# Kernel optimization log

Hardware: AMD Instinct MI355X
Metric: run time of the kernel (lower is better)

The kernel has to match this reference:

```python
import jax, jax.numpy as jnp
import numpy as np

B = 1024
FEATS = [("sirna_gibbs_energy", 19), ("pssm_score", 1), ("gc_sterch", 1), ("sirna_second_percent", 2), ("sirna_second_energy", 2), ("tri_nt_percent", 64), ("di_nt_percent", 16), ("single_nt_percent", 4), ("gc_content", 1)]
DFF = 2048  # torch TransformerEncoderLayer default dim_feedforward


def _posenc(S, d):
    pos = jnp.arange(S, dtype=jnp.float32)[:, None]
    div = jnp.exp(jnp.arange(0, d, 2, dtype=jnp.float32) * (-np.log(10000.0) / d))
    pe = jnp.zeros((S, d), jnp.float32)
    pe = pe.at[:, 0::2].set(jnp.sin(pos * div))
    pe = pe.at[:, 1::2].set(jnp.cos(pos * div))
    return pe


def _ln(x, g, b):
    m = x.mean(-1, keepdims=True)
    v = ((x - m) ** 2).mean(-1, keepdims=True)
    return (x - m) * jax.lax.rsqrt(v + 1e-5) * g + b


def _encoder_layer(x, qkv_w, qkv_b, ow, ob, f1w, f1b, f2w, f2b, g1, b1, g2, b2, nhead):
    Bx, S, d = x.shape
    dh = d // nhead
    qkv = jnp.einsum('bsd,ed->bse', x, qkv_w) + qkv_b  # [B,S,3d]
    q, k, v = jnp.split(qkv, 3, axis=-1)
    sh = lambda t: t.reshape(Bx, S, nhead, dh).transpose(0, 2, 1, 3)  # [B,h,S,dh]
    q, k, v = sh(q), sh(k), sh(v)
    att = jax.nn.softmax(jnp.einsum('bhqd,bhkd->bhqk', q, k) / np.sqrt(dh).astype(np.float32), axis=-1)
    o = jnp.einsum('bhqk,bhkd->bhqd', att, v).transpose(0, 2, 1, 3).reshape(Bx, S, d)
    o = o @ ow.T + ob
    x = _ln(x + o, g1, b1)  # post-norm (norm_first=False default)
    h = jax.nn.relu(x @ f1w.T + f1b) @ f2w.T + f2b
    return _ln(x + h, g2, b2)


def _encoder(x, qkv_w, qkv_b, ow, ob, f1w, f1b, f2w, f2b, g1, b1, g2, b2, nhead):
    for i in range(qkv_w.shape[0]):
        x = _encoder_layer(x, qkv_w[i], qkv_b[i], ow[i], ob[i], f1w[i], f1b[i], f2w[i], f2b[i], g1[i], b1[i], g2[i], b2[i], nhead)
    return x


def setup_inputs():
    key = jax.random.key(0)
    ks = iter(jax.random.split(key, 128))
    inp = {}
    inp['rnafm_encode'] = jax.random.normal(next(ks), (B, 21, 640), jnp.float32)
    inp['rnafm_encode_mrna'] = jax.random.normal(next(ks), (B, 59, 640), jnp.float32)
    for name, n in FEATS:
        inp[name] = jax.random.normal(next(ks), (B, n, 1), jnp.float32)

    def xav(shape):
        fan_out, fan_in = shape[-2], shape[-1]
        std = np.sqrt(2.0 / (fan_in + fan_out)).astype(np.float32)
        return jax.random.normal(next(ks), shape, jnp.float32) * std

    def enc_params(prefix, L, d):
        inp[prefix + '_qkv_w'] = xav((L, 3 * d, d))
        inp[prefix + '_qkv_b'] = jnp.zeros((L, 3 * d), jnp.float32)
        inp[prefix + '_ow'] = xav((L, d, d))
        inp[prefix + '_ob'] = jnp.zeros((L, d), jnp.float32)
        inp[prefix + '_f1w'] = xav((L, DFF, d))
        inp[prefix + '_f1b'] = jnp.zeros((L, DFF), jnp.float32)
        inp[prefix + '_f2w'] = xav((L, d, DFF))
        inp[prefix + '_f2b'] = jnp.zeros((L, d), jnp.float32)
        inp[prefix + '_g1'] = jnp.ones((L, d), jnp.float32)
        inp[prefix + '_b1'] = jnp.zeros((L, d), jnp.float32)
        inp[prefix + '_g2'] = jnp.ones((L, d), jnp.float32)
        inp[prefix + '_b2'] = jnp.zeros((L, d), jnp.float32)

    inp['xmap1_w'] = xav((16, 640)); inp['xmap1_b'] = jnp.zeros(16, jnp.float32)
    enc_params('enc1', 4, 16)
    inp['ymap1_w'] = xav((4, 16)); inp['ymap1_b'] = jnp.zeros(4, jnp.float32)
    inp['xmap2_w'] = xav((8, 640)); inp['xmap2_b'] = jnp.zeros(8, jnp.float32)
    enc_params('enc2', 2, 8)
    inp['ymap2_w'] = xav((1, 8)); inp['ymap2_b'] = jnp.zeros(1, jnp.float32)
    inp['bn_g'] = jnp.ones(253, jnp.float32); inp['bn_b'] = jnp.zeros(253, jnp.float32)
    inp['d1w'] = xav((256, 253)); inp['d1b'] = jnp.zeros(256, jnp.float32)
    inp['d2w'] = xav((64, 256)); inp['d2b'] = jnp.zeros(64, jnp.float32)
    inp['d3w'] = xav((16, 64)); inp['d3b'] = jnp.zeros(16, jnp.float32)
    inp['d4w'] = xav((1, 16)); inp['d4b'] = jnp.zeros(1, jnp.float32)
    return inp


def _forward(rnafm_encode, rnafm_encode_mrna, feats,
             xmap1_w, xmap1_b, enc1, ymap1_w, ymap1_b,
             xmap2_w, xmap2_b, enc2, ymap2_w, ymap2_b,
             bn_g, bn_b, d1w, d1b, d2w, d2b, d3w, d3b, d4w, d4b):
    # siRNA branch: [B,21,640] -> [B,21,16] -> encoder(4 layers, 2 heads) -> [B,21,4]
    x = rnafm_encode @ xmap1_w.T + xmap1_b
    x = x + _posenc(21, 16)
    x = _encoder(x, *enc1, nhead=2)
    as_att = (x @ ymap1_w.T + ymap1_b).reshape(x.shape[0], -1)  # [B,84]
    # mRNA branch: [B,59,640] -> [B,59,8] -> encoder(2 layers, 1 head) -> [B,59,1]
    y = rnafm_encode_mrna @ xmap2_w.T + xmap2_b
    y = y + _posenc(59, 8)
    y = _encoder(y, *enc2, nhead=1)
    mrna_att = (y @ ymap2_w.T + ymap2_b).reshape(y.shape[0], -1)  # [B,59]
    other = jnp.concatenate([f[..., 0] for f in feats], axis=1)  # [B,110]
    cat = jnp.concatenate([as_att, mrna_att, other], axis=1)  # [B,253]
    # BatchNorm1d in eval mode (running_mean=0, running_var=1, eps=1e-5)
    h = cat * jax.lax.rsqrt(jnp.float32(1.0 + 1e-5)) * bn_g + bn_b
    h = jax.nn.leaky_relu(h @ d1w.T + d1b, 0.01)
    h = jax.nn.leaky_relu(h @ d2w.T + d2b, 0.01)
    h = jax.nn.leaky_relu(h @ d3w.T + d3b, 0.01)
    out = jax.nn.sigmoid(h @ d4w.T + d4b)
    return out[:, 0]


def reference(rnafm_encode, rnafm_encode_mrna, sirna_gibbs_energy, pssm_score, gc_sterch,
              sirna_second_percent, sirna_second_energy, tri_nt_percent, di_nt_percent,
              single_nt_percent, gc_content,
              xmap1_w, xmap1_b,
              enc1_qkv_w, enc1_qkv_b, enc1_ow, enc1_ob, enc1_f1w, enc1_f1b, enc1_f2w, enc1_f2b,
              enc1_g1, enc1_b1, enc1_g2, enc1_b2,
              ymap1_w, ymap1_b,
              xmap2_w, xmap2_b,
              enc2_qkv_w, enc2_qkv_b, enc2_ow, enc2_ob, enc2_f1w, enc2_f1b, enc2_f2w, enc2_f2b,
              enc2_g1, enc2_b1, enc2_g2, enc2_b2,
              ymap2_w, ymap2_b,
              bn_g, bn_b, d1w, d1b, d2w, d2b, d3w, d3b, d4w, d4b):
    feats = (sirna_gibbs_energy, pssm_score, gc_sterch, sirna_second_percent,
             sirna_second_energy, tri_nt_percent, di_nt_percent, single_nt_percent, gc_content)
    enc1 = (enc1_qkv_w, enc1_qkv_b, enc1_ow, enc1_ob, enc1_f1w, enc1_f1b, enc1_f2w, enc1_f2b,
            enc1_g1, enc1_b1, enc1_g2, enc1_b2)
    enc2 = (enc2_qkv_w, enc2_qkv_b, enc2_ow, enc2_ob, enc2_f1w, enc2_f1b, enc2_f2w, enc2_f2b,
            enc2_g1, enc2_b1, enc2_g2, enc2_b2)
    return _forward(rnafm_encode, rnafm_encode_mrna, feats,
                    xmap1_w, xmap1_b, enc1, ymap1_w, ymap1_b,
                    xmap2_w, xmap2_b, enc2, ymap2_w, ymap2_b,
                    bn_g, bn_b, d1w, d1b, d2w, d2b, d3w, d3b, d4w, d4b)
```

## Files before the change

kernel.cpp:

```cpp
#include <hip/hip_runtime.h>
#include <math.h>

#define NB 1024

typedef __bf16 mbf8 __attribute__((ext_vector_type(8)));
typedef float  mf4  __attribute__((ext_vector_type(4)));

union Pk { __bf16 h[4]; uint2 u2; };

__device__ __forceinline__ mf4 mfma16(mbf8 a, mbf8 b, mf4 c) {
  return __builtin_amdgcn_mfma_f32_16x16x32_bf16(a, b, c, 0, 0, 0);
}

__device__ __forceinline__ float dot4f(float4 a, float4 b){
  return a.x*b.x + a.y*b.y + a.z*b.z + a.w*b.w;
}

__device__ __forceinline__ mbf8 ld_frag_f32(const float* p) {
  float4 u0 = *(const float4*)p;
  float4 u1 = *(const float4*)(p + 4);
  mbf8 v;
  v[0]=(__bf16)u0.x; v[1]=(__bf16)u0.y; v[2]=(__bf16)u0.z; v[3]=(__bf16)u0.w;
  v[4]=(__bf16)u1.x; v[5]=(__bf16)u1.y; v[6]=(__bf16)u1.z; v[7]=(__bf16)u1.w;
  return v;
}

__global__ __launch_bounds__(256) void prep_kernel(
    const float* __restrict__ xw1, const float* __restrict__ f1w1, const float* __restrict__ f2w1,
    const float* __restrict__ xw2, const float* __restrict__ f1w2, const float* __restrict__ f2w2,
    const float* __restrict__ d1w, const float* __restrict__ d2w, const float* __restrict__ d3w,
    __bf16* __restrict__ out)
{
  int idx = blockIdx.x * 256 + threadIdx.x;
  if (idx >= 693248) return;
  int which, local;
  if (idx < 10240)       { which = 0; local = idx; }
  else if (idx < 272384) { which = 1; local = idx - 10240; }
  else if (idx < 403456) { which = 2; local = idx - 272384; }
  else if (idx < 413696) { which = 3; local = idx - 403456; }
  else if (idx < 544768) { which = 4; local = idx - 413696; }
  else if (idx < 610304) { which = 5; local = idx - 544768; }
  else if (idx < 675840) { which = 6; local = idx - 610304; }
  else if (idx < 692224) { which = 7; local = idx - 675840; }
  else                   { which = 8; local = idx - 692224; }
  int tile = local >> 9, r = local & 511, lane = r >> 3, j = r & 7;
  int quad = lane >> 4, lm = lane & 15, khi = quad * 8 + j;
  float val = 0.f;
  switch (which) {
    case 0: { int k = tile*32 + khi; val = xw1[lm*640 + k]; } break;
    case 1: { int L = tile >> 7, nt = tile & 127, n = nt*16 + lm;
              val = (khi < 16) ? f1w1[(L*2048 + n)*16 + khi] : 0.f; } break;
    case 2: { int L = tile >> 6, ks = tile & 63, k = ks*32 + khi;
              val = f2w1[(L*16 + lm)*2048 + k]; } break;
    case 3: { int k = tile*32 + khi; val = (lm < 8) ? xw2[lm*640 + k] : 0.f; } break;
    case 4: { int L = tile >> 7, nt = tile & 127, n = nt*16 + lm;
              val = (khi < 8) ? f1w2[(L*2048 + n)*8 + khi] : 0.f; } break;
    case 5: { int L = tile >> 6, ks = tile & 63, k = ks*32 + khi;
              val = (lm < 8) ? f2w2[(L*8 + lm)*2048 + k] : 0.f; } break;
    case 6: { int nt = tile >> 3, ks = tile & 7, k = ks*32 + khi;
              val = (k < 253) ? d1w[(nt*16 + lm)*253 + k] : 0.f; } break;
    case 7: { int nt = tile >> 3, ks = tile & 7, k = ks*32 + khi;
              val = d2w[(nt*16 + lm)*256 + k]; } break;
    default:{ int ks = tile, k = ks*32 + khi;
              val = d3w[lm*64 + k]; } break;
  }
  out[idx] = (__bf16)val;
}

__global__ __launch_bounds__(256) void b1_kernel(
    const float* __restrict__ inp,
    const float* __restrict__ xb,
    const float* __restrict__ qw, const float* __restrict__ qb,
    const float* __restrict__ ow, const float* __restrict__ ob,
    const float* __restrict__ f1b, const float* __restrict__ f2b,
    const float* __restrict__ g1w, const float* __restrict__ b1w,
    const float* __restrict__ g2w, const float* __restrict__ b2w,
    const float* __restrict__ ymw, const float* __restrict__ ymb,
    const __bf16* __restrict__ xwB, const __bf16* __restrict__ w1B,
    const __bf16* __restrict__ w2B,
    float* __restrict__ outp)
{
  __shared__ __align__(16) float xs[21*20];
  __shared__ __align__(16) float xr[21*20];
  __shared__ __align__(16) float ao[21*20];
  __shared__ __align__(16) float pool[4288];
  __shared__ float mu[21], rsd[21];

  const int tid = threadIdx.x;
  const int b = blockIdx.x;
  const int w = tid >> 6, lane = tid & 63, quad = lane >> 4, lm = lane & 15;
  float* qkv = pool;
  float* sc  = pool + 1092;
  float* red = pool;
  __bf16* hbuf = (__bf16*)pool;
  const float* Ain = inp + (size_t)b * 21 * 640;

  mf4 pc0 = {0.f,0.f,0.f,0.f}, pc1 = {0.f,0.f,0.f,0.f};
  for (int i = 0; i < 5; ++i) {
    int ks = w*5 + i;
    mbf8 bv = *(const mbf8*)(xwB + (ks*64 + lane)*8);
    #pragma unroll
    for (int mt = 0; mt < 2; ++mt) {
      int row = mt*16 + lm; row = row > 20 ? 20 : row;
      mbf8 av = ld_frag_f32(Ain + row*640 + ks*32 + quad*8);
      if (mt == 0) pc0 = mfma16(av, bv, pc0); else pc1 = mfma16(av, bv, pc1);
    }
  }
  #pragma unroll
  for (int r = 0; r < 4; ++r) {
    red[((w*2+0)*16 + quad*4 + r)*17 + lm] = pc0[r];
    red[((w*2+1)*16 + quad*4 + r)*17 + lm] = pc1[r];
  }
  __syncthreads();
  {
    const float lf = -logf(10000.0f) / 16.0f;
    for (int idx = tid; idx < 336; idx += 256) {
      int t = idx >> 4, i = idx & 15, mt = t >> 4, tl = t & 15;
      float s = red[((0+mt)*16+tl)*17+i] + red[((2+mt)*16+tl)*17+i]
              + red[((4+mt)*16+tl)*17+i] + red[((6+mt)*16+tl)*17+i];
      float freq = expf((float)((i>>1)*2) * lf);
      float pe = (i & 1) ? cosf((float)t * freq) : sinf((float)t * freq);
      xs[t*20 + i] = s + xb[i] + pe;
    }
  }
  __syncthreads();

  for (int L = 0; L < 4; ++L) {
    for (int idx = tid; idx < 1008; idx += 256) {
      int s = idx / 48, e = idx % 48;
      const float* wr = qw + (L*48 + e)*16;
      float a = qb[L*48 + e];
      #pragma unroll
      for (int k = 0; k < 16; ++k) a += xs[s*20+k] * wr[k];
      qkv[s*52 + e] = a;
    }
    __syncthreads();

    for (int idx = tid; idx < 882; idx += 256) {
      int h = idx / 441, r2 = idx % 441, i = r2 / 21, j = r2 % 21;
      float4 q0 = *(const float4*)(qkv + i*52 + h*8);
      float4 q1 = *(const float4*)(qkv + i*52 + h*8 + 4);
      float4 k0 = *(const float4*)(qkv + j*52 + 16 + h*8);
      float4 k1 = *(const float4*)(qkv + j*52 + 16 + h*8 + 4);
      sc[(h*21 + i)*23 + j] = (dot4f(q0,k0) + dot4f(q1,k1)) * 0.35355339059327373f;
    }
    __syncthreads();

    {
      int r = tid >> 2, p = tid & 3;
      if (r < 42) {
        float* row = sc + r*23;
        float m = -1e30f;
        for (int j = p; j < 21; j += 4) m = fmaxf(m, row[j]);
        m = fmaxf(m, __shfl_xor(m, 1));
        m = fmaxf(m, __shfl_xor(m, 2));
        float ssum = 0.f;
        for (int j = p; j < 21; j += 4) { float e = __expf(row[j] - m); row[j] = e; ssum += e; }
        ssum += __shfl_xor(ssum, 1);
        ssum += __shfl_xor(ssum, 2);
        float inv = 1.f / ssum;
        for (int j = p; j < 21; j += 4) row[j] *= inv;
      }
    }
    __syncthreads();

    for (int idx = tid; idx < 336; idx += 256) {
      int s = idx >> 4, cc = idx & 15, h = cc >> 3, c = cc & 7;
      const float* row = sc + (h*21 + s)*23;
      float a = 0.f;
      for (int j = 0; j < 21; ++j) a += row[j] * qkv[j*52 + 32 + h*8 + c];
      ao[s*20 + cc] = a;
    }
    __syncthreads();

    for (int idx = tid; idx < 336; idx += 256) {
      int s = idx >> 4, i = idx & 15;
      const float* wr = ow + (L*16 + i)*16;
      float a = ob[L*16 + i];
      #pragma unroll
      for (int c = 0; c < 16; ++c) a += ao[s*20 + c] * wr[c];
      xr[s*20 + i] = xs[s*20 + i] + a;
    }
    __syncthreads();

    if (tid < 21) {
      float m = 0.f;
      #pragma unroll
      for (int k = 0; k < 16; ++k) m += xr[tid*20 + k];
      m *= (1.f/16.f);
      float v = 0.f;
      #pragma unroll
      for (int k = 0; k < 16; ++k) { float d = xr[tid*20 + k] - m; v += d*d; }
      v *= (1.f/16.f);
      mu[tid] = m; rsd[tid] = rsqrtf(v + 1e-5f);
    }
    __syncthreads();
    for (int idx = tid; idx < 336; idx += 256) {
      int s = idx >> 4, i = idx & 15;
      xs[s*20 + i] = (xr[s*20 + i] - mu[s]) * rsd[s] * g1w[L*16+i] + b1w[L*16+i];
    }
    __syncthreads();

    mbf8 xf0, xf1;
    {
      #pragma unroll
      for (int q = 0; q < 8; ++q) { xf0[q] = (__bf16)0.f; xf1[q] = (__bf16)0.f; }
      if (quad < 2) {
        int t0 = lm;
        int t1 = 16 + lm; if (t1 > 20) t1 = 20;
        xf0 = ld_frag_f32(xs + t0*20 + quad*8);
        xf1 = ld_frag_f32(xs + t1*20 + quad*8);
      }
    }
    mf4 of0 = {0.f,0.f,0.f,0.f}, of1 = {0.f,0.f,0.f,0.f};
    const __bf16* w1L = w1B + (size_t)L*128*512;
    const __bf16* w2L = w2B + (size_t)L*64*512;
    const float* f1bL = f1b + L*2048;
    for (int ci = 0; ci < 8; ++ci) {
      #pragma unroll
      for (int u = 0; u < 4; ++u) {
        int ut = ci*16 + w*4 + u;
        mbf8 wa = *(const mbf8*)(w1L + (ut*64 + lane)*8);
        float4 bia = *(const float4*)(f1bL + ut*16 + quad*4);
        mf4 z = {0.f,0.f,0.f,0.f};
        mf4 c0 = mfma16(wa, xf0, z);
        mf4 c1 = mfma16(wa, xf1, z);
        Pk p0, p1;
        p0.h[0]=(__bf16)fmaxf(c0[0]+bia.x,0.f); p0.h[1]=(__bf16)fmaxf(c0[1]+bia.y,0.f);
        p0.h[2]=(__bf16)fmaxf(c0[2]+bia.z,0.f); p0.h[3]=(__bf16)fmaxf(c0[3]+bia.w,0.f);
        p1.h[0]=(__bf16)fmaxf(c1[0]+bia.x,0.f); p1.h[1]=(__bf16)fmaxf(c1[1]+bia.y,0.f);
        p1.h[2]=(__bf16)fmaxf(c1[2]+bia.z,0.f); p1.h[3]=(__bf16)fmaxf(c1[3]+bia.w,0.f);
        int colb = (ut & 15)*16 + quad*4;
        *(uint2*)(hbuf + lm*268 + colb)        = p0.u2;
        *(uint2*)(hbuf + (16 + lm)*268 + colb) = p1.u2;
      }
      #pragma unroll
      for (int kk = 0; kk < 2; ++kk) {
        int ksl = w*2 + kk;
        mbf8 wb = *(const mbf8*)(w2L + ((ci*8 + ksl)*64 + lane)*8);
        mbf8 a0 = *(const mbf8*)(hbuf + lm*268 + ksl*32 + quad*8);
        mbf8 a1 = *(const mbf8*)(hbuf + (16 + lm)*268 + ksl*32 + quad*8);
        of0 = mfma16(a0, wb, of0);
        of1 = mfma16(a1, wb, of1);
      }
    }
    __syncthreads();
    #pragma unroll
    for (int r = 0; r < 4; ++r) {
      red[((w*2+0)*16 + quad*4 + r)*17 + lm] = of0[r];
      red[((w*2+1)*16 + quad*4 + r)*17 + lm] = of1[r];
    }
    __syncthreads();
    for (int idx = tid; idx < 336; idx += 256) {
      int t = idx >> 4, i = idx & 15, mt = t >> 4, tl = t & 15;
      float s = red[((0+mt)*16+tl)*17+i] + red[((2+mt)*16+tl)*17+i]
              + red[((4+mt)*16+tl)*17+i] + red[((6+mt)*16+tl)*17+i];
      xr[t*20 + i] = xs[t*20 + i] + s + f2b[L*16 + i];
    }
    __syncthreads();
    if (tid < 21) {
      float m = 0.f;
      #pragma unroll
      for (int k = 0; k < 16; ++k) m += xr[tid*20 + k];
      m *= (1.f/16.f);
      float v = 0.f;
      #pragma unroll
      for (int k = 0; k < 16; ++k) { float d = xr[tid*20 + k] - m; v += d*d; }
      v *= (1.f/16.f);
      mu[tid] = m; rsd[tid] = rsqrtf(v + 1e-5f);
    }
    __syncthreads();
    for (int idx = tid; idx < 336; idx += 256) {
      int s = idx >> 4, i = idx & 15;
      xs[s*20 + i] = (xr[s*20 + i] - mu[s]) * rsd[s] * g2w[L*16+i] + b2w[L*16+i];
    }
    __syncthreads();
  }

  for (int idx = tid; idx < 84; idx += 256) {
    int s = idx >> 2, j = idx & 3;
    float a = ymb[j];
    #pragma unroll
    for (int k = 0; k < 16; ++k) a += xs[s*20 + k] * ymw[j*16 + k];
    outp[(size_t)b*84 + idx] = a;
  }
}

__global__ __launch_bounds__(256) void b2_kernel(
    const float* __restrict__ inp,
    const float* __restrict__ xb,
    const float* __restrict__ qw, const float* __restrict__ qb,
    const float* __restrict__ ow, const float* __restrict__ ob,
    const float* __restrict__ f1b, const float* __restrict__ f2b,
    const float* __restrict__ g1w, const float* __restrict__ b1w,
    const float* __restrict__ g2w, const float* __restrict__ b2w,
    const float* __restrict__ ymw, const float* __restrict__ ymb,
    const __bf16* __restrict__ xwB, const __bf16* __restrict__ w1B,
    const __bf16* __restrict__ w2B,
    float* __restrict__ outp)
{
  __shared__ __align__(16) float xs[59*12];
  __shared__ __align__(16) float xr[59*12];
  __shared__ __align__(16) float ao[59*12];
  __shared__ __align__(16) float pool[5251];
  __shared__ float mu[59], rsd[59];

  const int tid = threadIdx.x;
  const int b = blockIdx.x;
  const int w = tid >> 6, lane = tid & 63, quad = lane >> 4, lm = lane & 15;
  float* qkv = pool;
  float* sc  = pool + 1652;
  float* red = pool;
  __bf16* hbuf = (__bf16*)pool;
  const float* Ain = inp + (size_t)b * 59 * 640;

  mf4 pc[4];
  #pragma unroll
  for (int mt = 0; mt < 4; ++mt) { mf4 z = {0.f,0.f,0.f,0.f}; pc[mt] = z; }
  for (int i = 0; i < 5; ++i) {
    int ks = w*5 + i;
    mbf8 bv = *(const mbf8*)(xwB + (ks*64 + lane)*8);
    #pragma unroll
    for (int mt = 0; mt < 4; ++mt) {
      int row = mt*16 + lm; row = row > 58 ? 58 : row;
      mbf8 av = ld_frag_f32(Ain + row*640 + ks*32 + quad*8);
      pc[mt] = mfma16(av, bv, pc[mt]);
    }
  }
  #pragma unroll
  for (int mt = 0; mt < 4; ++mt)
    #pragma unroll
    for (int r = 0; r < 4; ++r)
      red[((w*4+mt)*16 + quad*4 + r)*17 + lm] = pc[mt][r];
  __syncthreads();
  {
    const float lf = -logf(10000.0f) / 8.0f;
    for (int idx = tid; idx < 472; idx += 256) {
      int t = idx >> 3, i = idx & 7, mt = t >> 4, tl = t & 15;
      float s = red[((0*4+mt)*16+tl)*17+i] + red[((1*4+mt)*16+tl)*17+i]
              + red[((2*4+mt)*16+tl)*17+i] + red[((3*4+mt)*16+tl)*17+i];
      float freq = expf((float)((i>>1)*2) * lf);
      float pe = (i & 1) ? cosf((float)t * freq) : sinf((float)t * freq);
      xs[t*12 + i] = s + xb[i] + pe;
    }
  }
  __syncthreads();

  for (int L = 0; L < 2; ++L) {
    for (int idx = tid; idx < 1416; idx += 256) {
      int s = idx / 24, e = idx % 24;
      const float* wr = qw + (L*24 + e)*8;
      float a = qb[L*24 + e];
      #pragma unroll
      for (int k = 0; k < 8; ++k) a += xs[s*12+k] * wr[k];
      qkv[s*28 + e] = a;
    }
    __syncthreads();

    for (int idx = tid; idx < 3481; idx += 256) {
      int i = idx / 59, j = idx % 59;
      float4 q0 = *(const float4*)(qkv + i*28);
      float4 q1 = *(const float4*)(qkv + i*28 + 4);
      float4 k0 = *(const float4*)(qkv + j*28 + 8);
      float4 k1 = *(const float4*)(qkv + j*28 + 12);
      sc[i*61 + j] = (dot4f(q0,k0) + dot4f(q1,k1)) * 0.35355339059327373f;
    }
    __syncthreads();

    {
      int r = tid >> 2, p = tid & 3;
      if (r < 59) {
        float* row = sc + r*61;
        float m = -1e30f;
        for (int j = p; j < 59; j += 4) m = fmaxf(m, row[j]);
        m = fmaxf(m, __shfl_xor(m, 1));
        m = fmaxf(m, __shfl_xor(m, 2));
        float ssum = 0.f;
        for (int j = p; j < 59; j += 4) { float e = __expf(row[j] - m); row[j] = e; ssum += e; }
        ssum += __shfl_xor(ssum, 1);
        ssum += __shfl_xor(ssum, 2);
        float inv = 1.f / ssum;
        for (int j = p; j < 59; j += 4) row[j] *= inv;
      }
    }
    __syncthreads();

    for (int idx = tid; idx < 472; idx += 256) {
      int s = idx >> 3, c = idx & 7;
      const float* row = sc + s*61;
      float a = 0.f;
      for (int j = 0; j < 59; ++j) a += row[j] * qkv[j*28 + 16 + c];
      ao[s*12 + c] = a;
    }
    __syncthreads();

    for (int idx = tid; idx < 472; idx += 256) {
      int s = idx >> 3, i = idx & 7;
      const float* wr = ow + (L*8 + i)*8;
      float a = ob[L*8 + i];
      #pragma unroll
      for (int c = 0; c < 8; ++c) a += ao[s*12 + c] * wr[c];
      xr[s*12 + i] = xs[s*12 + i] + a;
    }
    __syncthreads();

    if (tid < 59) {
      float m = 0.f;
      #pragma unroll
      for (int k = 0; k < 8; ++k) m += xr[tid*12 + k];
      m *= 0.125f;
      float v = 0.f;
      #pragma unroll
      for (int k = 0; k < 8; ++k) { float d = xr[tid*12 + k] - m; v += d*d; }
      v *= 0.125f;
      mu[tid] = m; rsd[tid] = rsqrtf(v + 1e-5f);
    }
    __syncthreads();
    for (int idx = tid; idx < 472; idx += 256) {
      int s = idx >> 3, i = idx & 7;
      xs[s*12 + i] = (xr[s*12 + i] - mu[s]) * rsd[s] * g1w[L*8+i] + b1w[L*8+i];
    }
    __syncthreads();

    mbf8 xf[4];
    #pragma unroll
    for (int tt = 0; tt < 4; ++tt) {
      #pragma unroll
      for (int q = 0; q < 8; ++q) xf[tt][q] = (__bf16)0.f;
      if (quad == 0) {
        int tok = tt*16 + lm; if (tok > 58) tok = 58;
        xf[tt] = ld_frag_f32(xs + tok*12);
      }
    }
    mf4 of[4];
    #pragma unroll
    for (int mt = 0; mt < 4; ++mt) { mf4 z = {0.f,0.f,0.f,0.f}; of[mt] = z; }
    const __bf16* w1L = w1B + (size_t)L*128*512;
    const __bf16* w2L = w2B + (size_t)L*64*512;
    const float* f1bL = f1b + L*2048;
    for (int ci = 0; ci < 16; ++ci) {
      #pragma unroll
      for (int u = 0; u < 2; ++u) {
        int ut = ci*8 + w*2 + u;
        mbf8 wa = *(const mbf8*)(w1L + (ut*64 + lane)*8);
        float4 bia = *(const float4*)(f1bL + ut*16 + quad*4);
        int colb = (ut & 7)*16 + quad*4;
        #pragma unroll
        for (int tt = 0; tt < 4; ++tt) {
          mf4 z = {0.f,0.f,0.f,0.f};
          mf4 c = mfma16(wa, xf[tt], z);
          Pk p;
          p.h[0]=(__bf16)fmaxf(c[0]+bia.x,0.f); p.h[1]=(__bf16)fmaxf(c[1]+bia.y,0.f);
          p.h[2]=(__bf16)fmaxf(c[2]+bia.z,0.f); p.h[3]=(__bf16)fmaxf(c[3]+bia.w,0.f);
          *(uint2*)(hbuf + (tt*16 + lm)*140 + colb) = p.u2;
        }
      }
      {
        mbf8 wb = *(const mbf8*)(w2L + ((ci*4 + w)*64 + lane)*8);
        #pragma unroll
        for (int mt = 0; mt < 4; ++mt) {
          mbf8 ah = *(const mbf8*)(hbuf + (mt*16 + lm)*140 + w*32 + quad*8);
          of[mt] = mfma16(ah, wb, of[mt]);
        }
      }
    }
    __syncthreads();
    #pragma unroll
    for (int mt = 0; mt < 4; ++mt)
      #pragma unroll
      for (int r = 0; r < 4; ++r)
        red[((w*4+mt)*16 + quad*4 + r)*17 + lm] = of[mt][r];
    __syncthreads();
    for (int idx = tid; idx < 472; idx += 256) {
      int t = idx >> 3, i = idx & 7, mt = t >> 4, tl = t & 15;
      float s = red[((0*4+mt)*16+tl)*17+i] + red[((1*4+mt)*16+tl)*17+i]
              + red[((2*4+mt)*16+tl)*17+i] + red[((3*4+mt)*16+tl)*17+i];
      xr[t*12 + i] = xs[t*12 + i] + s + f2b[L*8 + i];
    }
    __syncthreads();
    if (tid < 59) {
      float m = 0.f;
      #pragma unroll
      for (int k = 0; k < 8; ++k) m += xr[tid*12 + k];
      m *= 0.125f;
      float v = 0.f;
      #pragma unroll
      for (int k = 0; k < 8; ++k) { float d = xr[tid*12 + k] - m; v += d*d; }
      v *= 0.125f;
      mu[tid] = m; rsd[tid] = rsqrtf(v + 1e-5f);
    }
    __syncthreads();
    for (int idx = tid; idx < 472; idx += 256) {
      int s = idx >> 3, i = idx & 7;
      xs[s*12 + i] = (xr[s*12 + i] - mu[s]) * rsd[s] * g2w[L*8+i] + b2w[L*8+i];
    }
    __syncthreads();
  }

  for (int s = tid; s < 59; s += 256) {
    float a = ymb[0];
    #pragma unroll
    for (int k = 0; k < 8; ++k) a += xs[s*12 + k] * ymw[k];
    outp[(size_t)b*59 + s] = a;
  }
}

__global__ __launch_bounds__(256) void mlp_kernel(
    const float* __restrict__ as_att, const float* __restrict__ mrna,
    const float* __restrict__ f_gibbs, const float* __restrict__ f_pssm,
    const float* __restrict__ f_gcs, const float* __restrict__ f_ssp,
    const float* __restrict__ f_sse, const float* __restrict__ f_tri,
    const float* __restrict__ f_di, const float* __restrict__ f_sgl,
    const float* __restrict__ f_gc,
    const float* __restrict__ bn_g, const float* __restrict__ bn_b,
    const float* __restrict__ d1b, const float* __restrict__ d2b,
    const float* __restrict__ d3b,
    const float* __restrict__ d4w, const float* __restrict__ d4b,
    const __bf16* __restrict__ d1B, const __bf16* __restrict__ d2B,
    const __bf16* __restrict__ d3B,
    float* __restrict__ outp)
{
  __shared__ __align__(16) float cat[16*268];
  __shared__ __align__(16) float h1[16*268];
  __shared__ __align__(16) float h2[16*68];
  __shared__ __align__(16) float h3[16*17];
  const int tid = threadIdx.x;
  const int bs  = blockIdx.x * 16;
  const int w = tid >> 6, lane = tid & 63, quad = lane >> 4, lm = lane & 15;
  const float bnscale = rsqrtf(1.0f + 1e-5f);

  for (int g = 0; g < 16; ++g) {
    int smp = bs + g;
    for (int j = tid; j < 253; j += 256) {
      float v;
      if (j < 84)       v = as_att[(size_t)smp*84 + j];
      else if (j < 143) v = mrna[(size_t)smp*59 + (j - 84)];
      else {
        int j2 = j - 143;
        if (j2 < 19)       v = f_gibbs[smp*19 + j2];
        else if (j2 < 20)  v = f_pssm[smp];
        else if (j2 < 21)  v = f_gcs[smp];
        else if (j2 < 23)  v = f_ssp[smp*2 + (j2-21)];
        else if (j2 < 25)  v = f_sse[smp*2 + (j2-23)];
        else if (j2 < 89)  v = f_tri[smp*64 + (j2-25)];
        else if (j2 < 105) v = f_di[smp*16 + (j2-89)];
        else if (j2 < 109) v = f_sgl[smp*4 + (j2-105)];
        else               v = f_gc[smp];
      }
      cat[g*268 + j] = v * bnscale * bn_g[j] + bn_b[j];
    }
  }
  if (tid < 48) { int g = tid / 3; cat[g*268 + 253 + tid % 3] = 0.f; }
  __syncthreads();

  {
    mf4 acc[4];
    #pragma unroll
    for (int q = 0; q < 4; ++q) { mf4 z = {0.f,0.f,0.f,0.f}; acc[q] = z; }
    for (int ks = 0; ks < 8; ++ks) {
      mbf8 af = ld_frag_f32(cat + lm*268 + ks*32 + quad*8);
      #pragma unroll
      for (int nt4 = 0; nt4 < 4; ++nt4) {
        int nt = w*4 + nt4;
        mbf8 bf = *(const mbf8*)(d1B + ((nt*8 + ks)*64 + lane)*8);
        acc[nt4] = mfma16(af, bf, acc[nt4]);
      }
    }
    #pragma unroll
    for (int nt4 = 0; nt4 < 4; ++nt4) {
      int n = (w*4 + nt4)*16 + lm;
      float bb = d1b[n];
      #pragma unroll
      for (int r = 0; r < 4; ++r) {
        float a = acc[nt4][r] + bb;
        h1[(quad*4 + r)*268 + n] = (a > 0.f) ? a : 0.01f * a;
      }
    }
  }
  __syncthreads();

  {
    mf4 acc = {0.f,0.f,0.f,0.f};
    for (int ks = 0; ks < 8; ++ks) {
      mbf8 af = ld_frag_f32(h1 + lm*268 + ks*32 + quad*8);
      mbf8 bf = *(const mbf8*)(d2B + ((w*8 + ks)*64 + lane)*8);
      acc = mfma16(af, bf, acc);
    }
    int n = w*16 + lm;
    float bb = d2b[n];
    #pragma unroll
    for (int r = 0; r < 4; ++r) {
      float a = acc[r] + bb;
      h2[(quad*4 + r)*68 + n] = (a > 0.f) ? a : 0.01f * a;
    }
  }
  __syncthreads();

  if (w == 0) {
    mf4 acc = {0.f,0.f,0.f,0.f};
    #pragma unroll
    for (int ks = 0; ks < 2; ++ks) {
      mbf8 af = ld_frag_f32(h2 + lm*68 + ks*32 + quad*8);
      mbf8 bf = *(const mbf8*)(d3B + (ks*64 + lane)*8);
      acc = mfma16(af, bf, acc);
    }
    float bb = d3b[lm];
    #pragma unroll
    for (int r = 0; r < 4; ++r) {
      float a = acc[r] + bb;
      h3[(quad*4 + r)*17 + lm] = (a > 0.f) ? a : 0.01f * a;
    }
  }
  __syncthreads();

  if (tid < 16) {
    float a = d4b[0];
    #pragma unroll
    for (int j = 0; j < 16; ++j) a += h3[tid*17 + j] * d4w[j];
    outp[bs + tid] = 1.f / (1.f + __expf(-a));
  }
}

extern "C" void kernel_launch(void* const* d_in, const int* in_sizes, int n_in,
                              void* d_out, int out_size, void* d_ws, size_t ws_size,
                              hipStream_t stream) {
  const float* rnafm   = (const float*)d_in[0];
  const float* rnafm_m = (const float*)d_in[1];
  const float* f_gibbs = (const float*)d_in[2];
  const float* f_pssm  = (const float*)d_in[3];
  const float* f_gcs   = (const float*)d_in[4];
  const float* f_ssp   = (const float*)d_in[5];
  const float* f_sse   = (const float*)d_in[6];
  const float* f_tri   = (const float*)d_in[7];
  const float* f_di    = (const float*)d_in[8];
  const float* f_sgl   = (const float*)d_in[9];
  const float* f_gc    = (const float*)d_in[10];
  const float* xmap1_w = (const float*)d_in[11];
  const float* xmap1_b = (const float*)d_in[12];
  const float* e1_qw   = (const float*)d_in[13];
  const float* e1_qb   = (const float*)d_in[14];
  const float* e1_ow   = (const float*)d_in[15];
  const float* e1_ob   = (const float*)d_in[16];
  const float* e1_f1w  = (const float*)d_in[17];
  const float* e1_f1b  = (const float*)d_in[18];
  const float* e1_f2w  = (const float*)d_in[19];
  const float* e1_f2b  = (const float*)d_in[20];
  const float* e1_g1   = (const float*)d_in[21];
  const float* e1_b1   = (const float*)d_in[22];
  const float* e1_g2   = (const float*)d_in[23];
  const float* e1_b2   = (const float*)d_in[24];
  const float* ymap1_w = (const float*)d_in[25];
  const float* ymap1_b = (const float*)d_in[26];
  const float* xmap2_w = (const float*)d_in[27];
  const float* xmap2_b = (const float*)d_in[28];
  const float* e2_qw   = (const float*)d_in[29];
  const float* e2_qb   = (const float*)d_in[30];
  const float* e2_ow   = (const float*)d_in[31];
  const float* e2_ob   = (const float*)d_in[32];
  const float* e2_f1w  = (const float*)d_in[33];
  const float* e2_f1b  = (const float*)d_in[34];
  const float* e2_f2w  = (const float*)d_in[35];
  const float* e2_f2b  = (const float*)d_in[36];
  const float* e2_g1   = (const float*)d_in[37];
  const float* e2_b1   = (const float*)d_in[38];
  const float* e2_g2   = (const float*)d_in[39];
  const float* e2_b2   = (const float*)d_in[40];
  const float* ymap2_w = (const float*)d_in[41];
  const float* ymap2_b = (const float*)d_in[42];
  const float* bn_g    = (const float*)d_in[43];
  const float* bn_b    = (const float*)d_in[44];
  const float* d1w     = (const float*)d_in[45];
  const float* d1b     = (const float*)d_in[46];
  const float* d2w     = (const float*)d_in[47];
  const float* d2b     = (const float*)d_in[48];
  const float* d3w     = (const float*)d_in[49];
  const float* d3b     = (const float*)d_in[50];
  const float* d4w     = (const float*)d_in[51];
  const float* d4b     = (const float*)d_in[52];

  float* as_att = (float*)d_ws;
  float* mrna   = (float*)((char*)d_ws + (size_t)NB*84*4);
  __bf16* bfb   = (__bf16*)((char*)d_ws + 585728);
  __bf16* xw1B  = bfb;
  __bf16* w1B1  = bfb + 10240;
  __bf16* w2B1  = bfb + 272384;
  __bf16* xw2B  = bfb + 403456;
  __bf16* w1B2  = bfb + 413696;
  __bf16* w2B2  = bfb + 544768;
  __bf16* d1B   = bfb + 610304;
  __bf16* d2B   = bfb + 675840;
  __bf16* d3B   = bfb + 692224;
  float* outp   = (float*)d_out;

  prep_kernel<<<2708, 256, 0, stream>>>(xmap1_w, e1_f1w, e1_f2w, xmap2_w, e2_f1w, e2_f2w,
                                        d1w, d2w, d3w, bfb);

  b1_kernel<<<NB, 256, 0, stream>>>(rnafm, xmap1_b,
      e1_qw, e1_qb, e1_ow, e1_ob, e1_f1b, e1_f2b,
      e1_g1, e1_b1, e1_g2, e1_b2, ymap1_w, ymap1_b,
      xw1B, w1B1, w2B1, as_att);

  b2_kernel<<<NB, 256, 0, stream>>>(rnafm_m, xmap2_b,
      e2_qw, e2_qb, e2_ow, e2_ob, e2_f1b, e2_f2b,
      e2_g1, e2_b1, e2_g2, e2_b2, ymap2_w, ymap2_b,
      xw2B, w1B2, w2B2, mrna);

  mlp_kernel<<<64, 256, 0, stream>>>(as_att, mrna,
      f_gibbs, f_pssm, f_gcs, f_ssp, f_sse, f_tri, f_di, f_sgl, f_gc,
      bn_g, bn_b, d1b, d2b, d3b, d4w, d4b, d1B, d2B, d3B, outp);
}
```

Before: 574.3 us.

## Merge both encoder kernels into one launch and use MFMA for attention

Fuses the two per-sample encoder kernels into one kernel with 2*NB blocks, where even blocks run encoder 1 and odd blocks run encoder 2 on a shared static LDS buffer. This removes one launch and lets the two workloads overlap across CUs. It also replaces the scalar QK^T and attention-times-V loops with bf16 16x16x32 MFMA ops. That lowers the precision of the attention scores and probabilities to bf16, and the larger merged LDS allocation may reduce occupancy for the smaller encoder.

```diff
diff --git a/kernel.cpp b/kernel.cpp
--- a/kernel.cpp
+++ b/kernel.cpp
@@ -22,6 +22,13 @@
   mbf8 v;
   v[0]=(__bf16)u0.x; v[1]=(__bf16)u0.y; v[2]=(__bf16)u0.z; v[3]=(__bf16)u0.w;
   v[4]=(__bf16)u1.x; v[5]=(__bf16)u1.y; v[6]=(__bf16)u1.z; v[7]=(__bf16)u1.w;
+  return v;
+}
+
+__device__ __forceinline__ mbf8 zero8() {
+  mbf8 v;
+  #pragma unroll
+  for (int q = 0; q < 8; ++q) v[q] = (__bf16)0.f;
   return v;
 }
 
@@ -67,9 +74,8 @@
   out[idx] = (__bf16)val;
 }
 
-__global__ __launch_bounds__(256) void b1_kernel(
-    const float* __restrict__ inp,
-    const float* __restrict__ xb,
+__device__ __forceinline__ void run_b1(int b, float* smem,
+    const float* __restrict__ inp, const float* __restrict__ xb,
     const float* __restrict__ qw, const float* __restrict__ qb,
     const float* __restrict__ ow, const float* __restrict__ ob,
     const float* __restrict__ f1b, const float* __restrict__ f2b,
@@ -77,17 +83,16 @@
     const float* __restrict__ g2w, const float* __restrict__ b2w,
     const float* __restrict__ ymw, const float* __restrict__ ymb,
     const __bf16* __restrict__ xwB, const __bf16* __restrict__ w1B,
-    const __bf16* __restrict__ w2B,
-    float* __restrict__ outp)
+    const __bf16* __restrict__ w2B, float* __restrict__ outp)
 {
-  __shared__ __align__(16) float xs[21*20];
-  __shared__ __align__(16) float xr[21*20];
-  __shared__ __align__(16) float ao[21*20];
-  __shared__ __align__(16) float pool[4288];
-  __shared__ float mu[21], rsd[21];
+  float* xs  = smem;
+  float* xr  = smem + 420;
+  float* ao  = smem + 840;
+  float* pool= smem + 1264;
+  float* mu  = smem + 5552;
+  float* rsd = smem + 5573;
 
   const int tid = threadIdx.x;
-  const int b = blockIdx.x;
   const int w = tid >> 6, lane = tid & 63, quad = lane >> 4, lm = lane & 15;
   float* qkv = pool;
   float* sc  = pool + 1092;
@@ -136,13 +141,32 @@
     }
     __syncthreads();
 
-    for (int idx = tid; idx < 882; idx += 256) {
-      int h = idx / 441, r2 = idx % 441, i = r2 / 21, j = r2 % 21;
-      float4 q0 = *(const float4*)(qkv + i*52 + h*8);
-      float4 q1 = *(const float4*)(qkv + i*52 + h*8 + 4);
-      float4 k0 = *(const float4*)(qkv + j*52 + 16 + h*8);
-      float4 k1 = *(const float4*)(qkv + j*52 + 16 + h*8 + 4);
-      sc[(h*21 + i)*23 + j] = (dot4f(q0,k0) + dot4f(q1,k1)) * 0.35355339059327373f;
+    {
+      int h = w >> 1, mt = w & 1;
+      mbf8 qf = zero8();
+      if (quad == 0) {
+        int tok = mt*16 + lm; tok = tok > 20 ? 20 : tok;
+        const float* p = qkv + tok*52 + h*8;
+        #pragma unroll
+        for (int j = 0; j < 8; ++j) qf[j] = (__bf16)(p[j] * 0.35355339059327373f);
+      }
+      #pragma unroll
+      for (int nt = 0; nt < 2; ++nt) {
+        mbf8 kf = zero8();
+        if (quad == 0) {
+          int key = nt*16 + lm; key = key > 20 ? 20 : key;
+          const float* p = qkv + key*52 + 16 + h*8;
+          #pragma unroll
+          for (int j = 0; j < 8; ++j) kf[j] = (__bf16)p[j];
+        }
+        mf4 z = {0.f,0.f,0.f,0.f};
+        mf4 c = mfma16(qf, kf, z);
+        #pragma unroll
+        for (int r = 0; r < 4; ++r) {
+          int row = mt*16 + quad*4 + r, col = nt*16 + lm;
+          if (row < 21 && col < 21) sc[(h*21 + row)*23 + col] = c[r];
+        }
+      }
     }
     __syncthreads();
 
@@ -164,12 +188,25 @@
     }
     __syncthreads();
 
-    for (int idx = tid; idx < 336; idx += 256) {
-      int s = idx >> 4, cc = idx & 15, h = cc >> 3, c = cc & 7;
-      const float* row = sc + (h*21 + s)*23;
-      float a = 0.f;
-      for (int j = 0; j < 21; ++j) a += row[j] * qkv[j*52 + 32 + h*8 + c];
-      ao[s*20 + cc] = a;
+    {
+      int h = w >> 1, mt = w & 1;
+      mbf8 pf = zero8(), vf = zero8();
+      {
+        int tok = mt*16 + lm;
+        #pragma unroll
+        for (int j = 0; j < 8; ++j) {
+          int k = quad*8 + j;
+          pf[j] = (__bf16)((tok < 21 && k < 21) ? sc[(h*21 + tok)*23 + k] : 0.f);
+          vf[j] = (__bf16)((lm < 8 && k < 21) ? qkv[k*52 + 32 + h*8 + lm] : 0.f);
+        }
+      }
+      mf4 z = {0.f,0.f,0.f,0.f};
+      mf4 c = mfma16(pf, vf, z);
+      #pragma unroll
+      for (int r = 0; r < 4; ++r) {
+        int tok = mt*16 + quad*4 + r;
+        if (tok < 21 && lm < 8) ao[tok*20 + h*8 + lm] = c[r];
+      }
     }
     __syncthreads();
 
@@ -201,16 +238,12 @@
     }
     __syncthreads();
 
-    mbf8 xf0, xf1;
-    {
-      #pragma unroll
-      for (int q = 0; q < 8; ++q) { xf0[q] = (__bf16)0.f; xf1[q] = (__bf16)0.f; }
-      if (quad < 2) {
-        int t0 = lm;
-        int t1 = 16 + lm; if (t1 > 20) t1 = 20;
-        xf0 = ld_frag_f32(xs + t0*20 + quad*8);
-        xf1 = ld_frag_f32(xs + t1*20 + quad*8);
-      }
+    mbf8 xf0 = zero8(), xf1 = zero8();
+    if (quad < 2) {
+      int t0 = lm;
+      int t1 = 16 + lm; if (t1 > 20) t1 = 20;
+      xf0 = ld_frag_f32(xs + t0*20 + quad*8);
+      xf1 = ld_frag_f32(xs + t1*20 + quad*8);
     }
     mf4 of0 = {0.f,0.f,0.f,0.f}, of1 = {0.f,0.f,0.f,0.f};
     const __bf16* w1L = w1B + (size_t)L*128*512;
@@ -286,9 +319,8 @@
   }
 }
 
-__global__ __launch_bounds__(256) void b2_kernel(
-    const float* __restrict__ inp,
-    const float* __restrict__ xb,
+__device__ __forceinline__ void run_b2(int b, float* smem,
+    const float* __restrict__ inp, const float* __restrict__ xb,
     const float* __restrict__ qw, const float* __restrict__ qb,
     const float* __restrict__ ow, const float* __restrict__ ob,
     const float* __restrict__ f1b, const float* __restrict__ f2b,
@@ -296,17 +328,16 @@
     const float* __restrict__ g2w, const float* __restrict__ b2w,
     const float* __restrict__ ymw, const float* __restrict__ ymb,
     const __bf16* __restrict__ xwB, const __bf16* __restrict__ w1B,
-    const __bf16* __restrict__ w2B,
-    float* __restrict__ outp)
+    const __bf16* __restrict__ w2B, float* __restrict__ outp)
 {
-  __shared__ __align__(16) float xs[59*12];
-  __shared__ __align__(16) float xr[59*12];
-  __shared__ __align__(16) float ao[59*12];
-  __shared__ __align__(16) float pool[5251];
-  __shared__ float mu[59], rsd[59];
+  float* xs  = smem;
+  float* xr  = smem + 708;
+  float* ao  = smem + 1416;
+  float* pool= smem + 2124;
+  float* mu  = smem + 7375;
+  float* rsd = smem + 7434;
 
   const int tid = threadIdx.x;
-  const int b = blockIdx.x;
   const int w = tid >> 6, lane = tid & 63, quad = lane >> 4, lm = lane & 15;
   float* qkv = pool;
   float* sc  = pool + 1652;
@@ -357,13 +388,31 @@
     }
     __syncthreads();
 
-    for (int idx = tid; idx < 3481; idx += 256) {
-      int i = idx / 59, j = idx % 59;
-      float4 q0 = *(const float4*)(qkv + i*28);
-      float4 q1 = *(const float4*)(qkv + i*28 + 4);
-      float4 k0 = *(const float4*)(qkv + j*28 + 8);
-      float4 k1 = *(const float4*)(qkv + j*28 + 12);
-      sc[i*61 + j] = (dot4f(q0,k0) + dot4f(q1,k1)) * 0.35355339059327373f;
+    {
+      mbf8 qf = zero8();
+      if (quad == 0) {
+        int tok = w*16 + lm; tok = tok > 58 ? 58 : tok;
+        const float* p = qkv + tok*28;
+        #pragma unroll
+        for (int j = 0; j < 8; ++j) qf[j] = (__bf16)(p[j] * 0.35355339059327373f);
+      }
+      #pragma unroll
+      for (int nt = 0; nt < 4; ++nt) {
+        mbf8 kf = zero8();
+        if (quad == 0) {
+          int key = nt*16 + lm; key = key > 58 ? 58 : key;
+          const float* p = qkv + key*28 + 8;
+          #pragma unroll
+          for (int j = 0; j < 8; ++j) kf[j] = (__bf16)p[j];
+        }
+        mf4 z = {0.f,0.f,0.f,0.f};
+        mf4 c = mfma16(qf, kf, z);
+        #pragma unroll
+        for (int r = 0; r < 4; ++r) {
+          int row = w*16 + quad*4 + r, col = nt*16 + lm;
+          if (row < 59 && col < 59) sc[row*61 + col] = c[r];
+        }
+      }
     }
     __syncthreads();
 
@@ -385,12 +434,25 @@
     }
     __syncthreads();
 
-    for (int idx = tid; idx < 472; idx += 256) {
-      int s = idx >> 3, c = idx & 7;
-      const float* row = sc + s*61;
-      float a = 0.f;
-      for (int j = 0; j < 59; ++j) a += row[j] * qkv[j*28 + 16 + c];
-      ao[s*12 + c] = a;
+    {
+      mf4 acc = {0.f,0.f,0.f,0.f};
+      #pragma unroll
+      for (int kk = 0; kk < 2; ++kk) {
+        mbf8 pf = zero8(), vf = zero8();
+        int tok = w*16 + lm;
+        #pragma unroll
+        for (int j = 0; j < 8; ++j) {
+          int k = kk*32 + quad*8 + j;
+          pf[j] = (__bf16)((tok < 59 && k < 59) ? sc[tok*61 + k] : 0.f);
+          vf[j] = (__bf16)((lm < 8 && k < 59) ? qkv[k*28 + 16 + lm] : 0.f);
+        }
+        acc = mfma16(pf, vf, acc);
+      }
+      #pragma unroll
+      for (int r = 0; r < 4; ++r) {
+        int tok = w*16 + quad*4 + r;
+        if (tok < 59 && lm < 8) ao[tok*12 + lm] = acc[r];
+      }
     }
     __syncthreads();
 
@@ -425,8 +487,7 @@
     mbf8 xf[4];
     #pragma unroll
     for (int tt = 0; tt < 4; ++tt) {
-      #pragma unroll
-      for (int q = 0; q < 8; ++q) xf[tt][q] = (__bf16)0.f;
+      xf[tt] = zero8();
       if (quad == 0) {
         int tok = tt*16 + lm; if (tok > 58) tok = 58;
         xf[tt] = ld_frag_f32(xs + tok*12);
@@ -502,6 +563,40 @@
     #pragma unroll
     for (int k = 0; k < 8; ++k) a += xs[s*12 + k] * ymw[k];
     outp[(size_t)b*59 + s] = a;
+  }
+}
+
+__global__ __launch_bounds__(256) void enc_kernel(
+    const float* __restrict__ inp1, const float* __restrict__ inp2,
+    const float* __restrict__ xb1,
+    const float* __restrict__ qw1, const float* __restrict__ qb1,
+    const float* __restrict__ ow1, const float* __restrict__ ob1,
+    const float* __restrict__ f1b1, const float* __restrict__ f2b1,
+    const float* __restrict__ g1w1, const float* __restrict__ b1w1,
+    const float* __restrict__ g2w1, const float* __restrict__ b2w1,
+    const float* __restrict__ ymw1, const float* __restrict__ ymb1,
+    const __bf16* __restrict__ xw1B, const __bf16* __restrict__ w1B1,
+    const __bf16* __restrict__ w2B1,
+    const float* __restrict__ xb2,
+    const float* __restrict__ qw2, const float* __restrict__ qb2,
+    const float* __restrict__ ow2, const float* __restrict__ ob2,
+    const float* __restrict__ f1b2, const float* __restrict__ f2b2,
+    const float* __restrict__ g1w2, const float* __restrict__ b1w2,
+    const float* __restrict__ g2w2, const float* __restrict__ b2w2,
+    const float* __restrict__ ymw2, const float* __restrict__ ymb2,
+    const __bf16* __restrict__ xw2B, const __bf16* __restrict__ w1B2,
+    const __bf16* __restrict__ w2B2,
+    float* __restrict__ as_att, float* __restrict__ mrna)
+{
+  __shared__ __align__(16) float smem[7600];
+  int bid = blockIdx.x;
+  int b = bid >> 1;
+  if ((bid & 1) == 0) {
+    run_b1(b, smem, inp1, xb1, qw1, qb1, ow1, ob1, f1b1, f2b1,
+           g1w1, b1w1, g2w1, b2w1, ymw1, ymb1, xw1B, w1B1, w2B1, as_att);
+  } else {
+    run_b2(b, smem, inp2, xb2, qw2, qb2, ow2, ob2, f1b2, f2b2,
+           g1w2, b1w2, g2w2, b2w2, ymw2, ymb2, xw2B, w1B2, w2B2, mrna);
   }
 }
 
@@ -695,15 +790,12 @@
   prep_kernel<<<2708, 256, 0, stream>>>(xmap1_w, e1_f1w, e1_f2w, xmap2_w, e2_f1w, e2_f2w,
                                         d1w, d2w, d3w, bfb);
 
-  b1_kernel<<<NB, 256, 0, stream>>>(rnafm, xmap1_b,
-      e1_qw, e1_qb, e1_ow, e1_ob, e1_f1b, e1_f2b,
-      e1_g1, e1_b1, e1_g2, e1_b2, ymap1_w, ymap1_b,
-      xw1B, w1B1, w2B1, as_att);
-
-  b2_kernel<<<NB, 256, 0, stream>>>(rnafm_m, xmap2_b,
-      e2_qw, e2_qb, e2_ow, e2_ob, e2_f1b, e2_f2b,
-      e2_g1, e2_b1, e2_g2, e2_b2, ymap2_w, ymap2_b,
-      xw2B, w1B2, w2B2, mrna);
+  enc_kernel<<<2*NB, 256, 0, stream>>>(rnafm, rnafm_m,
+      xmap1_b, e1_qw, e1_qb, e1_ow, e1_ob, e1_f1b, e1_f2b,
+      e1_g1, e1_b1, e1_g2, e1_b2, ymap1_w, ymap1_b, xw1B, w1B1, w2B1,
+      xmap2_b, e2_qw, e2_qb, e2_ow, e2_ob, e2_f1b, e2_f2b,
+      e2_g1, e2_b1, e2_g2, e2_b2, ymap2_w, ymap2_b, xw2B, w1B2, w2B2,
+      as_att, mrna);
 
   mlp_kernel<<<64, 256, 0, stream>>>(as_att, mrna,
       f_gibbs, f_pssm, f_gcs, f_ssp, f_sse, f_tri, f_di, f_sgl, f_gc,
```

Result: slower. 593.5 us (+3.3%).
